# Kernel tuning notes

Measured on AMD Instinct MI355X. Metric: run time of the kernel, lower is better.

## Reference

```python
import jax, jax.numpy as jnp
import numpy as np

N, K, H, E, HEADS, MULT = 10000, 32, 128, 128, 8, 2
HD = H // HEADS


def _ln(x, g, b):
    m = jnp.mean(x, axis=-1, keepdims=True)
    v = jnp.var(x, axis=-1, keepdims=True)
    return (x - m) * jax.lax.rsqrt(v + 1e-5) * g + b


def setup_inputs() -> dict:
    key = jax.random.key(0)
    ks = jax.random.split(key, 40)
    s = 0.05
    inp = {
        "node_features": jax.random.normal(ks[0], (N, H), jnp.float32),
        "edge_features": jax.random.normal(ks[1], (N, K, H), jnp.float32),
        "edge_attr": jax.random.normal(ks[2], (N, K, E), jnp.float32),
        "neighbor_list": jax.random.randint(ks[3], (N, K), 0, N),
        "num_valid": jax.random.randint(ks[4], (N,), 1, K + 1),
        # edge_linear: E -> H (with activation)
        "W_edge": jax.random.normal(ks[5], (E, H), jnp.float32) * s,
        "b_edge": jnp.zeros((H,), jnp.float32),
        # node_linear: 2H -> H (cat of center + gathered neighbor features)
        "W_node": jax.random.normal(ks[6], (2 * H, H), jnp.float32) * s,
        "b_node": jnp.zeros((H,), jnp.float32),
        # message_linear: 2H -> H
        "W_msg": jax.random.normal(ks[7], (2 * H, H), jnp.float32) * s,
        "b_msg": jnp.zeros((H,), jnp.float32),
        # multi-head attention in/out projections
        "W_qkv": jax.random.normal(ks[8], (H, 3 * H), jnp.float32) * s,
        "b_qkv": jnp.zeros((3 * H,), jnp.float32),
        "W_out": jax.random.normal(ks[9], (H, H), jnp.float32) * s,
        "b_out": jnp.zeros((H,), jnp.float32),
        # layernorms
        "g_attn": jnp.ones((H,), jnp.float32), "be_attn": jnp.zeros((H,), jnp.float32),
        "g_fn": jnp.ones((H,), jnp.float32), "be_fn": jnp.zeros((H,), jnp.float32),
        "g_fe": jnp.ones((H,), jnp.float32), "be_fe": jnp.zeros((H,), jnp.float32),
        # FFNs (node and edge), hidden = MULT*H
        "Wn1": jax.random.normal(ks[10], (H, MULT * H), jnp.float32) * s,
        "bn1": jnp.zeros((MULT * H,), jnp.float32),
        "Wn2": jax.random.normal(ks[11], (MULT * H, H), jnp.float32) * s,
        "bn2": jnp.zeros((H,), jnp.float32),
        "We1": jax.random.normal(ks[12], (H, MULT * H), jnp.float32) * s,
        "be1": jnp.zeros((MULT * H,), jnp.float32),
        "We2": jax.random.normal(ks[13], (MULT * H, H), jnp.float32) * s,
        "be2": jnp.zeros((H,), jnp.float32),
    }
    return inp


def _block(node_features, edge_features, edge_attr, neighbor_list, mask,
           W_edge, b_edge, W_node, b_node, W_msg, b_msg,
           W_qkv, b_qkv, W_out, b_out,
           g_attn, be_attn, g_fn, be_fn, g_fe, be_fe,
           Wn1, bn1, Wn2, bn2, We1, be1, We2, be2):
    act = jax.nn.gelu
    # --- pre-attention norm on nodes ---
    node_hidden = _ln(node_features, g_attn, be_attn)                 # [N,H]
    # --- graph attention: gather -> MLPs -> local windowed attention -> scatter ---
    edge_hidden = act(jnp.einsum('nke,eh->nkh', edge_attr, W_edge) + b_edge)   # [N,K,H]
    nbr = node_hidden[neighbor_list]                                   # [N,K,H] gather
    center = jnp.broadcast_to(node_hidden[:, None, :], nbr.shape)      # [N,K,H]
    node_cat = jnp.concatenate([center, nbr], axis=-1)                 # [N,K,2H]
    node_hid = act(jnp.einsum('nkf,fh->nkh', node_cat, W_node) + b_node)
    msg = act(jnp.einsum('nkf,fh->nkh',
                         jnp.concatenate([edge_hidden, node_hid], axis=-1),
                         W_msg) + b_msg)                               # [N,K,H]
    # multi-head self-attention per node over its K neighbors, key padding mask
    qkv = jnp.einsum('nkh,hf->nkf', msg, W_qkv) + b_qkv                # [N,K,3H]
    q, k, v = jnp.split(qkv, 3, axis=-1)
    q = q.reshape(N, K, HEADS, HD)
    k = k.reshape(N, K, HEADS, HD)
    v = v.reshape(N, K, HEADS, HD)
    scores = jnp.einsum('nqhd,nkhd->nhqk', q, k) / np.sqrt(HD)         # [N,heads,K,K]
    scores = jnp.where(mask[:, None, None, :], scores, jnp.float32(-1e9))
    attn = jax.nn.softmax(scores, axis=-1)
    ctx = jnp.einsum('nhqk,nkhd->nqhd', attn, v).reshape(N, K, H)
    edge_out = jnp.einsum('nkh,hf->nkf', ctx, W_out) + b_out           # [N,K,H]
    # masked scatter-aggregate back to nodes
    node_out = jnp.sum(edge_out * mask[:, :, None], axis=1)            # [N,H]
    # residuals
    node_features = node_out + node_features
    edge_features = edge_out + edge_features
    # --- FFN block ---
    nh = _ln(node_features, g_fn, be_fn)
    eh = _ln(edge_features, g_fe, be_fe)
    nh = act(nh @ Wn1 + bn1) @ Wn2 + bn2
    eh = jnp.einsum('nkf,fh->nkh', act(jnp.einsum('nkh,hf->nkf', eh, We1) + be1), We2) + be2
    return node_features + nh, edge_features + eh


def reference(node_features, edge_features, edge_attr, neighbor_list, num_valid,
              W_edge, b_edge, W_node, b_node, W_msg, b_msg,
              W_qkv, b_qkv, W_out, b_out,
              g_attn, be_attn, g_fn, be_fn, g_fe, be_fe,
              Wn1, bn1, Wn2, bn2, We1, be1, We2, be2):
    mask = jnp.arange(K)[None, :] < num_valid[:, None]                 # [N,K] bool
    return _block(node_features, edge_features, edge_attr, neighbor_list, mask,
                  W_edge, b_edge, W_node, b_node, W_msg, b_msg,
                  W_qkv, b_qkv, W_out, b_out,
                  g_attn, be_attn, g_fn, be_fn, g_fe, be_fe,
                  Wn1, bn1, Wn2, bn2, We1, be1, We2, be2)
```

## Files before the change

### kernel.cpp

```cpp
#include <hip/hip_runtime.h>
#include <hip/hip_bf16.h>
#include <cstddef>

#define N_NODES 10000
#define KNBR 32
#define HDIM 128
#define NHEADS 8

using short8 = __attribute__((ext_vector_type(8))) short;
using short4v = __attribute__((ext_vector_type(4))) short;
using f32x4 = __attribute__((ext_vector_type(4))) float;

__device__ __forceinline__ f32x4 mfma16(short8 a, short8 b, f32x4 c) {
  return __builtin_amdgcn_mfma_f32_16x16x32_bf16(a, b, c, 0, 0, 0);
}

__device__ __forceinline__ short f2bf(float f) {
  __hip_bfloat16 h = __float2bfloat16(f);
  return __builtin_bit_cast(short, h);
}
__device__ __forceinline__ float bf2f(short s) {
  unsigned u = ((unsigned)(unsigned short)s) << 16;
  return __builtin_bit_cast(float, u);
}

__device__ __forceinline__ float gelu_f(float x) {
  float a = 0.7978845608028654f * fmaf(0.044715f * x, x * x, x);
  float e = __expf(2.0f * a);
  return 0.5f * x * (2.0f - 2.0f / (e + 1.0f));
}

__device__ __forceinline__ short4v pack4f(float a, float b, float c, float d) {
  short4v v; v[0] = f2bf(a); v[1] = f2bf(b); v[2] = f2bf(c); v[3] = f2bf(d);
  return v;
}
__device__ __forceinline__ short4v pack_gelu4(f32x4 acc, float4 bb) {
  return pack4f(gelu_f(acc[0] + bb.x), gelu_f(acc[1] + bb.y),
                gelu_f(acc[2] + bb.z), gelu_f(acc[3] + bb.w));
}

__device__ __forceinline__ short8 ld_sw128(const short* b, int r, int ch) {
  return *(const short8*)(b + r * 128 + (((ch ^ (r & 7))) << 3));
}
__device__ __forceinline__ short8 ld_sw256(const short* b, int r, int ch) {
  return *(const short8*)(b + r * 256 + (((ch ^ (r & 7))) << 3));
}
__device__ __forceinline__ void st_sw128(short* b, int r, int col, short v) {
  b[r * 128 + ((((col >> 3) ^ (r & 7))) << 3) + (col & 7)] = v;
}
__device__ __forceinline__ void st_sw128_v4(short* b, int r, int colb, short4v v) {
  *(short4v*)(b + r * 128 + ((((colb >> 3) ^ (r & 7))) << 3) + (colb & 7)) = v;
}
__device__ __forceinline__ void st_sw256_v4(short* b, int r, int colb, short4v v) {
  *(short4v*)(b + r * 256 + ((((colb >> 3) ^ (r & 7))) << 3) + (colb & 7)) = v;
}

template <int MT, int NT, int KS, typename ALoad, typename Epi>
__device__ __forceinline__ void wgemm(ALoad aload, const short* __restrict__ Bt,
                                      Epi epi) {
  const int lane = threadIdx.x & 63;
  const int lm = lane & 15, lq = lane >> 4;
  short8 a[MT][KS];
#pragma unroll
  for (int mt = 0; mt < MT; ++mt)
#pragma unroll
    for (int k = 0; k < KS; ++k) a[mt][k] = aload(mt * 16 + lm, k, lq);
#pragma unroll
  for (int nt = 0; nt < NT; ++nt) {
    short8 b[KS];
#pragma unroll
    for (int k = 0; k < KS; ++k)
      b[k] = *(const short8*)(Bt + (nt * 16 + lm) * (KS * 32) + k * 32 + lq * 8);
#pragma unroll
    for (int mt = 0; mt < MT; ++mt) {
      f32x4 acc = {0.f, 0.f, 0.f, 0.f};
#pragma unroll
      for (int k = 0; k < KS; ++k) acc = mfma16(a[mt][k], b[k], acc);
      epi(mt, nt, acc);
    }
  }
}

template <int MT, int NT, int KS, typename ALoad, typename Epi>
__device__ __forceinline__ void wgemm_t(ALoad aload, const short* __restrict__ Bt,
                                        Epi epi) {
  const int lane = threadIdx.x & 63;
  const int lm = lane & 15, lq = lane >> 4;
  short8 a[MT][KS];
#pragma unroll
  for (int mt = 0; mt < MT; ++mt)
#pragma unroll
    for (int k = 0; k < KS; ++k) a[mt][k] = aload(mt * 16 + lm, k, lq);
#pragma unroll
  for (int nt = 0; nt < NT; ++nt) {
    short8 b[KS];
#pragma unroll
    for (int k = 0; k < KS; ++k)
      b[k] = *(const short8*)(Bt + (nt * 16 + lm) * (KS * 32) + k * 32 + lq * 8);
#pragma unroll
    for (int mt = 0; mt < MT; ++mt) {
      f32x4 acc = {0.f, 0.f, 0.f, 0.f};
#pragma unroll
      for (int k = 0; k < KS; ++k) acc = mfma16(b[k], a[mt][k], acc);
      epi(mt, nt, acc);
    }
  }
}

struct WSrc { const float* p[9]; };

__global__ void wprep_kernel(WSrc ws, short* __restrict__ dst) {
  const int cum[10] = {0, 16384, 49152, 81920, 131072, 147456, 180224, 212992, 245760, 278528};
  const int Ks[9] = {128, 256, 256, 128, 128, 128, 256, 128, 256};
  const int Ns[9] = {128, 128, 128, 384, 128, 256, 128, 256, 128};
  int eg = blockIdx.x * 256 + threadIdx.x;
  int id = 0;
#pragma unroll
  for (int i = 0; i < 8; ++i) id += (eg >= cum[i + 1]) ? 1 : 0;
  int e = eg - cum[id];
  int K = Ks[id];
  int n = (K == 128) ? (e >> 7) : (e >> 8);
  int k = e - n * K;
  dst[eg] = f2bf(ws.p[id][k * Ns[id] + n]);
}

__global__ __launch_bounds__(256) void ln_in_kernel(
    const float* __restrict__ in, const float* __restrict__ g,
    const float* __restrict__ be, short* __restrict__ out) {
  __shared__ float scr[32 * 8 * 2 + 64];
  const int tid = threadIdx.x;
  const int r = tid >> 3, j = tid & 7;
  const int base = blockIdx.x * 32;
  const int rg = base + r;
  const bool valid = rg < N_NODES;
  float4 v[4];
#pragma unroll
  for (int i = 0; i < 4; ++i)
    v[i] = valid ? ((const float4*)(in + (size_t)rg * 128 + j * 16))[i]
                 : make_float4(0.f, 0.f, 0.f, 0.f);
  float s = 0.f, s2 = 0.f;
#pragma unroll
  for (int i = 0; i < 4; ++i) {
    s += v[i].x + v[i].y + v[i].z + v[i].w;
    s2 = fmaf(v[i].x, v[i].x, s2); s2 = fmaf(v[i].y, v[i].y, s2);
    s2 = fmaf(v[i].z, v[i].z, s2); s2 = fmaf(v[i].w, v[i].w, s2);
  }
  scr[r * 8 + j] = s;
  scr[256 + r * 8 + j] = s2;
  __syncthreads();
  if (tid < 32) {
    float ss = 0.f, q2 = 0.f;
#pragma unroll
    for (int i = 0; i < 8; ++i) { ss += scr[tid * 8 + i]; q2 += scr[256 + tid * 8 + i]; }
    float mn = ss * (1.f / 128.f);
    float vr = fmaf(-mn, mn, q2 * (1.f / 128.f));
    scr[512 + tid] = mn;
    scr[544 + tid] = rsqrtf(vr + 1e-5f);
  }
  __syncthreads();
  if (!valid) return;
  float mn = scr[512 + r], rs = scr[544 + r];
  short8 o[2];
#pragma unroll
  for (int i = 0; i < 4; ++i) {
    int c0 = j * 16 + i * 4;
    float4 gg = *(const float4*)(g + c0);
    float4 bb = *(const float4*)(be + c0);
    float* vf = (float*)&v[i];
    float* gf = (float*)&gg;
    float* bf = (float*)&bb;
#pragma unroll
    for (int e = 0; e < 4; ++e)
      o[i >> 1][(i & 1) * 4 + e] = f2bf(fmaf((vf[e] - mn) * rs, gf[e], bf[e]));
  }
  *(short8*)(out + (size_t)rg * 128 + j * 16) = o[0];
  *(short8*)(out + (size_t)rg * 128 + j * 16 + 8) = o[1];
}

__global__ __launch_bounds__(256, 3) void egab_main(
    const float* __restrict__ nf, const float* __restrict__ ef,
    const float* __restrict__ ea, const int* __restrict__ nlist,
    const int* __restrict__ nvalid,
    const float* __restrict__ b_edge, const float* __restrict__ b_node,
    const float* __restrict__ b_msg, const float* __restrict__ b_qkv,
    const float* __restrict__ b_out, const float* __restrict__ g_fe,
    const float* __restrict__ be_fe, const float* __restrict__ be1,
    const float* __restrict__ be2,
    const short* __restrict__ WtE, const short* __restrict__ WtN,
    const short* __restrict__ WtM, const short* __restrict__ WtQ,
    const short* __restrict__ WtO, const short* __restrict__ WtE1,
    const short* __restrict__ WtE2, const short* __restrict__ nh_bf,
    float* __restrict__ out_node, float* __restrict__ out_edge) {
  __shared__ short lds[16384];
  short* R0 = lds;
  short* R1 = lds + 4096;
  short* R2 = lds + 8192;
  short* R3 = lds + 12288;

  const int tid = threadIdx.x;
  const int w = tid >> 6;
  const int lane = tid & 63;
  const int lm = lane & 15, lq = lane >> 4;
  const int base = blockIdx.x;
  const int n0 = w * 32;

  float efr[2][2][4];
  float nfr[2];
#pragma unroll
  for (int mt = 0; mt < 2; ++mt)
#pragma unroll
    for (int nt = 0; nt < 2; ++nt)
#pragma unroll
      for (int rr = 0; rr < 4; ++rr)
        efr[mt][nt][rr] =
            ef[((size_t)base * KNBR + mt * 16 + lq * 4 + rr) * 128 + n0 +
               nt * 16 + lm];
#pragma unroll
  for (int nt = 0; nt < 2; ++nt)
    nfr[nt] = nf[(size_t)base * 128 + n0 + nt * 16 + lm];

  {
    const float* eap = ea + (size_t)base * 4096;
    int r = tid >> 3;
    int sg = tid & 7;
#pragma unroll
    for (int j = 0; j < 2; ++j) {
      int ch = sg * 2 + j;
      float4 fa = ((const float4*)eap)[r * 32 + ch * 2];
      float4 fb = ((const float4*)eap)[r * 32 + ch * 2 + 1];
      short8 v = {f2bf(fa.x), f2bf(fa.y), f2bf(fa.z), f2bf(fa.w),
                  f2bf(fb.x), f2bf(fb.y), f2bf(fb.z), f2bf(fb.w)};
      *(short8*)(R0 + r * 128 + ((ch ^ (r & 7)) << 3)) = v;
    }
    int idx = nlist[base * KNBR + r];
    const short* srow = nh_bf + (size_t)idx * 128;
#pragma unroll
    for (int j = 0; j < 2; ++j) {
      int ch = sg * 2 + j;
      short8 v = *(const short8*)(srow + ch * 8);
      *(short8*)(R1 + r * 128 + ((ch ^ (r & 7)) << 3)) = v;
    }
  }
  __syncthreads();

  wgemm_t<2, 2, 4>(
      [&](int r, int k, int q) { return ld_sw128(R0, r, k * 4 + q); },
      WtE + (size_t)n0 * 128,
      [&](int mt, int nt, f32x4 acc) {
        int colb = n0 + nt * 16 + lq * 4;
        float4 bb = *(const float4*)(b_edge + colb);
        st_sw128_v4(R2, mt * 16 + lm, colb, pack_gelu4(acc, bb));
      });
  wgemm_t<2, 2, 8>(
      [&](int r, int k, int q) {
        if (k < 4)
          return *(const short8*)(nh_bf + (size_t)base * 128 + k * 32 + q * 8);
        return ld_sw128(R1, r, (k - 4) * 4 + q);
      },
      WtN + (size_t)n0 * 256,
      [&](int mt, int nt, f32x4 acc) {
        int colb = n0 + nt * 16 + lq * 4;
        float4 bb = *(const float4*)(b_node + colb);
        st_sw128_v4(R3, mt * 16 + lm, colb, pack_gelu4(acc, bb));
      });
  __syncthreads();

  wgemm_t<2, 2, 8>(
      [&](int r, int k, int q) {
        if (k < 4) return ld_sw128(R2, r, k * 4 + q);
        return ld_sw128(R3, r, (k - 4) * 4 + q);
      },
      WtM + (size_t)n0 * 256,
      [&](int mt, int nt, f32x4 acc) {
        int colb = n0 + nt * 16 + lq * 4;
        float4 bb = *(const float4*)(b_msg + colb);
        st_sw128_v4(R0, mt * 16 + lm, colb, pack_gelu4(acc, bb));
      });
  __syncthreads();

  {
    const int q0 = w * 96;
    wgemm<2, 6, 4>(
        [&](int r, int k, int q) { return ld_sw128(R0, r, k * 4 + q); },
        WtQ + (size_t)q0 * 128,
        [&](int mt, int nt, f32x4 acc) {
          int c = q0 + nt * 16;
          float bb = b_qkv[c + lm];
          int m = mt * 16 + lq * 4;
          if (c < 256) {
            short* dst = (c < 128 ? R1 + ((c >> 4) * 32) * 16
                                  : R2 + (((c - 128) >> 4) * 32) * 16);
#pragma unroll
            for (int rr = 0; rr < 4; ++rr)
              dst[(m + rr) * 16 + lm] = f2bf(acc[rr] + bb);
          } else {
            int rv = (c - 256) + lm;
            short4v pv;
#pragma unroll
            for (int rr = 0; rr < 4; ++rr) pv[rr] = f2bf(acc[rr] + bb);
            int chv = m >> 3;
            *(short4v*)(R3 + rv * 32 + ((chv ^ (rv & 3)) << 3) + (m & 7)) = pv;
          }
        });
  }
  __syncthreads();

  {
    const short8 zz = {0, 0, 0, 0, 0, 0, 0, 0};
    const f32x4 z4 = {0.f, 0.f, 0.f, 0.f};
    const int nvv = nvalid[base];
#pragma unroll
    for (int it = 0; it < 2; ++it) {
      int h = (it << 2) | w;
      short* qh = R1 + h * 512;
      short* kh = R2 + h * 512;
      short8 bk[2];
#pragma unroll
      for (int nt = 0; nt < 2; ++nt)
        bk[nt] = (lq < 2) ? *(const short8*)(kh + (nt * 16 + lm) * 16 + lq * 8) : zz;
      float sc[2][2][4];
#pragma unroll
      for (int mt = 0; mt < 2; ++mt) {
        short8 aq = (lq < 2) ? *(const short8*)(qh + (mt * 16 + lm) * 16 + lq * 8) : zz;
#pragma unroll
        for (int nt = 0; nt < 2; ++nt) {
          f32x4 s = mfma16(aq, bk[nt], z4);
#pragma unroll
          for (int rr = 0; rr < 4; ++rr) {
            float x = s[rr] * 0.25f;
            if (nt * 16 + lm >= nvv) x = -1e9f;
            sc[mt][nt][rr] = x;
          }
        }
      }
#pragma unroll
      for (int mt = 0; mt < 2; ++mt)
#pragma unroll
        for (int rr = 0; rr < 4; ++rr) {
          float x0 = sc[mt][0][rr], x1 = sc[mt][1][rr];
          float mx = fmaxf(x0, x1);
          mx = fmaxf(mx, __shfl_xor(mx, 1, 16));
          mx = fmaxf(mx, __shfl_xor(mx, 2, 16));
          mx = fmaxf(mx, __shfl_xor(mx, 4, 16));
          mx = fmaxf(mx, __shfl_xor(mx, 8, 16));
          float e0 = __expf(x0 - mx), e1 = __expf(x1 - mx);
          float sm = e0 + e1;
          sm += __shfl_xor(sm, 1, 16);
          sm += __shfl_xor(sm, 2, 16);
          sm += __shfl_xor(sm, 4, 16);
          sm += __shfl_xor(sm, 8, 16);
          float ri = 1.f / sm;
          int row = mt * 16 + lq * 4 + rr;
          qh[row * 16 + lm] = f2bf(e0 * ri);
          kh[row * 16 + lm] = f2bf(e1 * ri);
        }
#pragma unroll
      for (int mt = 0; mt < 2; ++mt) {
        const short* psrc = (lq < 2) ? qh : kh;
        short8 pa = *(const short8*)(psrc + (mt * 16 + lm) * 16 + (lq & 1) * 8);
        int rv = h * 16 + lm;
        short8 vb = *(const short8*)(R3 + rv * 32 + ((lq ^ (rv & 3)) << 3));
        f32x4 c = mfma16(pa, vb, z4);
#pragma unroll
        for (int rr = 0; rr < 4; ++rr)
          st_sw128(R0, mt * 16 + lq * 4 + rr, h * 16 + lm, f2bf(c[rr]));
      }
    }
  }
  __syncthreads();

  {
    int nv = nvalid[base];
    float nsum[2] = {0.f, 0.f};
    wgemm<2, 2, 4>(
        [&](int r, int k, int q) { return ld_sw128(R0, r, k * 4 + q); },
        WtO + (size_t)n0 * 128,
        [&](int mt, int nt, f32x4 acc) {
          int col = n0 + nt * 16 + lm;
          float bb = b_out[col];
#pragma unroll
          for (int rr = 0; rr < 4; ++rr) {
            int kk = mt * 16 + lq * 4 + rr;
            float eo = acc[rr] + bb;
            if (kk < nv) nsum[nt] += eo;
            st_sw128(R1, kk, col, f2bf(eo + efr[mt][nt][rr]));
          }
        });
#pragma unroll
    for (int nt = 0; nt < 2; ++nt) {
      float v = nsum[nt];
      v += __shfl_xor(v, 16, 64);
      v += __shfl_xor(v, 32, 64);
      if (lq == 0) {
        int col = n0 + nt * 16 + lm;
        out_node[(size_t)base * 128 + col] = v + nfr[nt];
      }
    }
  }
  __syncthreads();

  {
    float* scr = (float*)R2;
    int r = tid >> 3, sg = tid & 7;
    short8 xv[2];
    float s = 0.f, s2 = 0.f;
#pragma unroll
    for (int j = 0; j < 2; ++j) {
      int ch = sg * 2 + j;
      xv[j] = *(const short8*)(R1 + r * 128 + ((ch ^ (r & 7)) << 3));
#pragma unroll
      for (int e = 0; e < 8; ++e) {
        float x = bf2f(xv[j][e]);
        s += x;
        s2 = fmaf(x, x, s2);
      }
    }
    scr[r * 8 + sg] = s;
    scr[256 + r * 8 + sg] = s2;
    __syncthreads();
    if (tid < 32) {
      float ss = 0.f, q2 = 0.f;
#pragma unroll
      for (int i = 0; i < 8; ++i) { ss += scr[tid * 8 + i]; q2 += scr[256 + tid * 8 + i]; }
      float mn = ss * (1.f / 128.f);
      float vr = fmaf(-mn, mn, q2 * (1.f / 128.f));
      scr[512 + tid * 2] = mn;
      scr[512 + tid * 2 + 1] = rsqrtf(vr + 1e-5f);
    }
    __syncthreads();
    float mn = scr[512 + r * 2], rs = scr[512 + r * 2 + 1];
#pragma unroll
    for (int j = 0; j < 2; ++j) {
      int ch = sg * 2 + j;
      int c0 = ch * 8;
      float4 g0 = *(const float4*)(g_fe + c0);
      float4 g1 = *(const float4*)(g_fe + c0 + 4);
      float4 b0 = *(const float4*)(be_fe + c0);
      float4 b1 = *(const float4*)(be_fe + c0 + 4);
      const float* gp0 = (const float*)&g0;
      const float* gp1 = (const float*)&g1;
      const float* bp0 = (const float*)&b0;
      const float* bp1 = (const float*)&b1;
      short8 ov;
#pragma unroll
      for (int e = 0; e < 4; ++e) {
        ov[e] = f2bf(fmaf((bf2f(xv[j][e]) - mn) * rs, gp0[e], bp0[e]));
        ov[4 + e] = f2bf(fmaf((bf2f(xv[j][4 + e]) - mn) * rs, gp1[e], bp1[e]));
      }
      *(short8*)(R0 + r * 128 + ((ch ^ (r & 7)) << 3)) = ov;
    }
  }
  __syncthreads();

  {
    const int f0 = w * 64;
    wgemm_t<2, 4, 4>(
        [&](int r, int k, int q) { return ld_sw128(R0, r, k * 4 + q); },
        WtE1 + (size_t)f0 * 128,
        [&](int mt, int nt, f32x4 acc) {
          int colb = f0 + nt * 16 + lq * 4;
          float4 bb = *(const float4*)(be1 + colb);
          st_sw256_v4(R2, mt * 16 + lm, colb, pack_gelu4(acc, bb));
        });
  }
  __syncthreads();

  wgemm<2, 2, 8>(
      [&](int r, int k, int q) { return ld_sw256(R2, r, k * 4 + q); },
      WtE2 + (size_t)n0 * 256,
      [&](int mt, int nt, f32x4 acc) {
        int col = n0 + nt * 16 + lm;
        float bb = be2[col];
#pragma unroll
        for (int rr = 0; rr < 4; ++rr) {
          int m = mt * 16 + lq * 4 + rr;
          float rv = bf2f(R1[m * 128 + ((((col >> 3) ^ (m & 7))) << 3) + (col & 7)]);
          out_edge[((size_t)base * KNBR + m) * 128 + col] = rv + acc[rr] + bb;
        }
      });
}

__global__ __launch_bounds__(256, 4) void node_ffn_kernel(
    const float* __restrict__ nres, const float* __restrict__ g,
    const float* __restrict__ be, const short* __restrict__ WtN1,
    const float* __restrict__ bn1, const short* __restrict__ WtN2,
    const float* __restrict__ bn2, float* __restrict__ out) {
  __shared__ short lds[8192];
  short* EHN = lds;
  float* scr = (float*)(lds + 2048);
  short* HID = lds + 4096;

  const int tid = threadIdx.x;
  const int w = tid >> 6;
  const int lane = tid & 63;
  const int lm = lane & 15, lq = lane >> 4;
  const int base = blockIdx.x * 16;
  const int n0 = w * 32;

  {
    int r = tid >> 4, sg = tid & 15;
    bool valid = (base + r) < N_NODES;
    float xf[8];
#pragma unroll
    for (int i = 0; i < 2; ++i) {
      float4 v = valid ? ((const float4*)(nres + (size_t)(base + r) * 128 + sg * 8))[i]
                       : make_float4(0.f, 0.f, 0.f, 0.f);
      xf[i * 4] = v.x; xf[i * 4 + 1] = v.y; xf[i * 4 + 2] = v.z; xf[i * 4 + 3] = v.w;
    }
    float s = 0.f, s2 = 0.f;
#pragma unroll
    for (int i = 0; i < 8; ++i) { s += xf[i]; s2 = fmaf(xf[i], xf[i], s2); }
    scr[r * 16 + sg] = s;
    scr[256 + r * 16 + sg] = s2;
    __syncthreads();
    if (tid < 16) {
      float ss = 0.f, q2 = 0.f;
#pragma unroll
      for (int i = 0; i < 16; ++i) { ss += scr[tid * 16 + i]; q2 += scr[256 + tid * 16 + i]; }
      float mn = ss * (1.f / 128.f);
      float vr = fmaf(-mn, mn, q2 * (1.f / 128.f));
      scr[512 + tid * 2] = mn;
      scr[512 + tid * 2 + 1] = rsqrtf(vr + 1e-5f);
    }
    __syncthreads();
    float mn = scr[512 + r * 2], rs = scr[512 + r * 2 + 1];
    int c0 = sg * 8;
    short8 ov;
#pragma unroll
    for (int e = 0; e < 8; ++e)
      ov[e] = f2bf(fmaf((xf[e] - mn) * rs, g[c0 + e], be[c0 + e]));
    *(short8*)(EHN + r * 128 + ((sg ^ (r & 7)) << 3)) = ov;
  }
  __syncthreads();

  {
    const int f0 = w * 64;
    wgemm_t<1, 4, 4>(
        [&](int r, int k, int q) { return ld_sw128(EHN, r, k * 4 + q); },
        WtN1 + (size_t)f0 * 128,
        [&](int mt, int nt, f32x4 acc) {
          int colb = f0 + nt * 16 + lq * 4;
          float4 bb = *(const float4*)(bn1 + colb);
          st_sw256_v4(HID, mt * 16 + lm, colb, pack_gelu4(acc, bb));
        });
  }
  __syncthreads();

  wgemm<1, 2, 8>(
      [&](int r, int k, int q) { return ld_sw256(HID, r, k * 4 + q); },
      WtN2 + (size_t)n0 * 256,
      [&](int mt, int nt, f32x4 acc) {
        int col = n0 + nt * 16 + lm;
        float bb = bn2[col];
#pragma unroll
        for (int rr = 0; rr < 4; ++rr) {
          int m = mt * 16 + lq * 4 + rr;
          if (base + m < N_NODES) {
            float rv = nres[(size_t)(base + m) * 128 + col];
            out[(size_t)(base + m) * 128 + col] = rv + acc[rr] + bb;
          }
        }
      });
}

extern "C" void kernel_launch(void* const* d_in, const int* in_sizes, int n_in,
                              void* d_out, int out_size, void* d_ws,
                              size_t ws_size, hipStream_t stream) {
  (void)in_sizes; (void)n_in; (void)out_size; (void)ws_size;
  const float* nf = (const float*)d_in[0];
  const float* ef = (const float*)d_in[1];
  const float* ea = (const float*)d_in[2];
  const int* nlist = (const int*)d_in[3];
  const int* nvalid = (const int*)d_in[4];
  const float* W_edge = (const float*)d_in[5];
  const float* b_edge = (const float*)d_in[6];
  const float* W_node = (const float*)d_in[7];
  const float* b_node = (const float*)d_in[8];
  const float* W_msg = (const float*)d_in[9];
  const float* b_msg = (const float*)d_in[10];
  const float* W_qkv = (const float*)d_in[11];
  const float* b_qkv = (const float*)d_in[12];
  const float* W_out = (const float*)d_in[13];
  const float* b_out = (const float*)d_in[14];
  const float* g_attn = (const float*)d_in[15];
  const float* be_attn = (const float*)d_in[16];
  const float* g_fn = (const float*)d_in[17];
  const float* be_fn = (const float*)d_in[18];
  const float* g_fe = (const float*)d_in[19];
  const float* be_fe = (const float*)d_in[20];
  const float* Wn1 = (const float*)d_in[21];
  const float* bn1 = (const float*)d_in[22];
  const float* Wn2 = (const float*)d_in[23];
  const float* bn2 = (const float*)d_in[24];
  const float* We1 = (const float*)d_in[25];
  const float* be1 = (const float*)d_in[26];
  const float* We2 = (const float*)d_in[27];
  const float* be2 = (const float*)d_in[28];

  short* ws0 = (short*)d_ws;
  short* wsW = ws0 + 1280000;
  short* WtE = wsW;
  short* WtN = wsW + 16384;
  short* WtM = wsW + 49152;
  short* WtQ = wsW + 81920;
  short* WtO = wsW + 131072;
  short* WtE1 = wsW + 147456;
  short* WtE2 = wsW + 180224;
  short* WtN1 = wsW + 212992;
  short* WtN2 = wsW + 245760;

  float* out_node = (float*)d_out;
  float* out_edge = out_node + (size_t)N_NODES * 128;

  WSrc wsrc;
  wsrc.p[0] = W_edge; wsrc.p[1] = W_node; wsrc.p[2] = W_msg;
  wsrc.p[3] = W_qkv;  wsrc.p[4] = W_out;  wsrc.p[5] = We1;
  wsrc.p[6] = We2;    wsrc.p[7] = Wn1;    wsrc.p[8] = Wn2;

  wprep_kernel<<<1088, 256, 0, stream>>>(wsrc, wsW);
  ln_in_kernel<<<(N_NODES + 31) / 32, 256, 0, stream>>>(nf, g_attn, be_attn, ws0);
  egab_main<<<N_NODES, 256, 0, stream>>>(
      nf, ef, ea, nlist, nvalid, b_edge, b_node, b_msg, b_qkv, b_out, g_fe,
      be_fe, be1, be2, WtE, WtN, WtM, WtQ, WtO, WtE1, WtE2, ws0, out_node,
      out_edge);
  node_ffn_kernel<<<(N_NODES + 15) / 16, 256, 0, stream>>>(
      out_node, g_fn, be_fn, WtN1, bn1, WtN2, bn2, out_node);
}
```

Baseline: 911.8 us.

## Fuse node FFN into main kernel and use cheaper sigmoid-form GELU

Removes the separate node_ffn_kernel launch. Each block of egab_main now computes the node LayerNorm and runs the node FFN for its single node, using MFMA with only row 0 of the A operand non-zero. GELU is rewritten as x*sigmoid(1.5958*(x+0.044715x^3)), using hardware exp2 and rcp intrinsics to cut transcendental cost. The trade-off is wasted MFMA work on padded rows, extra weight loads per block (WtN1/WtN2 read by all 10000 blocks), and slightly more LDS use.

Measured after the change: 1.023 ms. 12.1% more time.

```diff
diff --git a/kernel.cpp b/kernel.cpp
--- a/kernel.cpp
+++ b/kernel.cpp
@@ -25,9 +25,8 @@
 }
 
 __device__ __forceinline__ float gelu_f(float x) {
-  float a = 0.7978845608028654f * fmaf(0.044715f * x, x * x, x);
-  float e = __expf(2.0f * a);
-  return 0.5f * x * (2.0f - 2.0f / (e + 1.0f));
+  float u = x * fmaf(x * x, -0.1029432f, -2.3022077f);
+  return x * __builtin_amdgcn_rcpf(1.0f + __builtin_amdgcn_exp2f(u));
 }
 
 __device__ __forceinline__ short4v pack4f(float a, float b, float c, float d) {
@@ -185,17 +184,21 @@
     const float* __restrict__ b_msg, const float* __restrict__ b_qkv,
     const float* __restrict__ b_out, const float* __restrict__ g_fe,
     const float* __restrict__ be_fe, const float* __restrict__ be1,
-    const float* __restrict__ be2,
+    const float* __restrict__ be2, const float* __restrict__ g_fn,
+    const float* __restrict__ be_fn, const float* __restrict__ bn1,
+    const float* __restrict__ bn2,
     const short* __restrict__ WtE, const short* __restrict__ WtN,
     const short* __restrict__ WtM, const short* __restrict__ WtQ,
     const short* __restrict__ WtO, const short* __restrict__ WtE1,
-    const short* __restrict__ WtE2, const short* __restrict__ nh_bf,
+    const short* __restrict__ WtE2, const short* __restrict__ WtN1,
+    const short* __restrict__ WtN2, const short* __restrict__ nh_bf,
     float* __restrict__ out_node, float* __restrict__ out_edge) {
-  __shared__ short lds[16384];
+  __shared__ short lds[16384 + 384];
   short* R0 = lds;
   short* R1 = lds + 4096;
   short* R2 = lds + 8192;
   short* R3 = lds + 12288;
+  short* ffn = lds + 16384;
 
   const int tid = threadIdx.x;
   const int w = tid >> 6;
@@ -203,6 +206,9 @@
   const int lm = lane & 15, lq = lane >> 4;
   const int base = blockIdx.x;
   const int n0 = w * 32;
+  const short8 zz8 = {0, 0, 0, 0, 0, 0, 0, 0};
+
+  float xres[2];
 
   float efr[2][2][4];
   float nfr[2];
@@ -306,7 +312,6 @@
   __syncthreads();
 
   {
-    const short8 zz = {0, 0, 0, 0, 0, 0, 0, 0};
     const f32x4 z4 = {0.f, 0.f, 0.f, 0.f};
     const int nvv = nvalid[base];
 #pragma unroll
@@ -317,11 +322,11 @@
       short8 bk[2];
 #pragma unroll
       for (int nt = 0; nt < 2; ++nt)
-        bk[nt] = (lq < 2) ? *(const short8*)(kh + (nt * 16 + lm) * 16 + lq * 8) : zz;
+        bk[nt] = (lq < 2) ? *(const short8*)(kh + (nt * 16 + lm) * 16 + lq * 8) : zz8;
       float sc[2][2][4];
 #pragma unroll
       for (int mt = 0; mt < 2; ++mt) {
-        short8 aq = (lq < 2) ? *(const short8*)(qh + (mt * 16 + lm) * 16 + lq * 8) : zz;
+        short8 aq = (lq < 2) ? *(const short8*)(qh + (mt * 16 + lm) * 16 + lq * 8) : zz8;
 #pragma unroll
         for (int nt = 0; nt < 2; ++nt) {
           f32x4 s = mfma16(aq, bk[nt], z4);
@@ -386,15 +391,14 @@
             st_sw128(R1, kk, col, f2bf(eo + efr[mt][nt][rr]));
           }
         });
+    float* xf = (float*)R2;
 #pragma unroll
     for (int nt = 0; nt < 2; ++nt) {
       float v = nsum[nt];
       v += __shfl_xor(v, 16, 64);
       v += __shfl_xor(v, 32, 64);
-      if (lq == 0) {
-        int col = n0 + nt * 16 + lm;
-        out_node[(size_t)base * 128 + col] = v + nfr[nt];
-      }
+      xres[nt] = v + nfr[nt];
+      if (lq == 0) xf[1024 + n0 + nt * 16 + lm] = xres[nt];
     }
   }
   __syncthreads();
@@ -417,6 +421,12 @@
     }
     scr[r * 8 + sg] = s;
     scr[256 + r * 8 + sg] = s2;
+    if (tid < 32) {
+      float4 x4 = *(const float4*)(scr + 1024 + tid * 4);
+      scr[832 + tid] = x4.x + x4.y + x4.z + x4.w;
+      scr[864 + tid] = fmaf(x4.x, x4.x, fmaf(x4.y, x4.y,
+                       fmaf(x4.z, x4.z, x4.w * x4.w)));
+    }
     __syncthreads();
     if (tid < 32) {
       float ss = 0.f, q2 = 0.f;
@@ -426,6 +436,14 @@
       float vr = fmaf(-mn, mn, q2 * (1.f / 128.f));
       scr[512 + tid * 2] = mn;
       scr[512 + tid * 2 + 1] = rsqrtf(vr + 1e-5f);
+    } else if (tid == 64) {
+      float ss = 0.f, q2 = 0.f;
+#pragma unroll
+      for (int i = 0; i < 32; ++i) { ss += scr[832 + i]; q2 += scr[864 + i]; }
+      float mn = ss * (1.f / 128.f);
+      float vr = fmaf(-mn, mn, q2 * (1.f / 128.f));
+      scr[896] = mn;
+      scr[897] = rsqrtf(vr + 1e-5f);
     }
     __syncthreads();
     float mn = scr[512 + r * 2], rs = scr[512 + r * 2 + 1];
@@ -449,6 +467,10 @@
       }
       *(short8*)(R0 + r * 128 + ((ch ^ (r & 7)) << 3)) = ov;
     }
+    if (tid < 128) {
+      float mx = scr[896], rx = scr[897];
+      ffn[tid] = f2bf(fmaf((scr[1024 + tid] - mx) * rx, g_fn[tid], be_fn[tid]));
+    }
   }
   __syncthreads();
 
@@ -462,6 +484,19 @@
           float4 bb = *(const float4*)(be1 + colb);
           st_sw256_v4(R2, mt * 16 + lm, colb, pack_gelu4(acc, bb));
         });
+    wgemm<1, 4, 4>(
+        [&](int r, int k, int q) {
+          short8 av = *(const short8*)(ffn + k * 32 + q * 8);
+          return (lm == 0) ? av : zz8;
+        },
+        WtN1 + (size_t)f0 * 128,
+        [&](int mt, int nt, f32x4 acc) {
+          (void)mt;
+          if (lq == 0) {
+            int col = f0 + nt * 16 + lm;
+            ffn[128 + col] = f2bf(gelu_f(acc[0] + bn1[col]));
+          }
+        });
   }
   __syncthreads();
 
@@ -478,87 +513,17 @@
           out_edge[((size_t)base * KNBR + m) * 128 + col] = rv + acc[rr] + bb;
         }
       });
-}
-
-__global__ __launch_bounds__(256, 4) void node_ffn_kernel(
-    const float* __restrict__ nres, const float* __restrict__ g,
-    const float* __restrict__ be, const short* __restrict__ WtN1,
-    const float* __restrict__ bn1, const short* __restrict__ WtN2,
-    const float* __restrict__ bn2, float* __restrict__ out) {
-  __shared__ short lds[8192];
-  short* EHN = lds;
-  float* scr = (float*)(lds + 2048);
-  short* HID = lds + 4096;
-
-  const int tid = threadIdx.x;
-  const int w = tid >> 6;
-  const int lane = tid & 63;
-  const int lm = lane & 15, lq = lane >> 4;
-  const int base = blockIdx.x * 16;
-  const int n0 = w * 32;
-
-  {
-    int r = tid >> 4, sg = tid & 15;
-    bool valid = (base + r) < N_NODES;
-    float xf[8];
-#pragma unroll
-    for (int i = 0; i < 2; ++i) {
-      float4 v = valid ? ((const float4*)(nres + (size_t)(base + r) * 128 + sg * 8))[i]
-                       : make_float4(0.f, 0.f, 0.f, 0.f);
-      xf[i * 4] = v.x; xf[i * 4 + 1] = v.y; xf[i * 4 + 2] = v.z; xf[i * 4 + 3] = v.w;
-    }
-    float s = 0.f, s2 = 0.f;
-#pragma unroll
-    for (int i = 0; i < 8; ++i) { s += xf[i]; s2 = fmaf(xf[i], xf[i], s2); }
-    scr[r * 16 + sg] = s;
-    scr[256 + r * 16 + sg] = s2;
-    __syncthreads();
-    if (tid < 16) {
-      float ss = 0.f, q2 = 0.f;
-#pragma unroll
-      for (int i = 0; i < 16; ++i) { ss += scr[tid * 16 + i]; q2 += scr[256 + tid * 16 + i]; }
-      float mn = ss * (1.f / 128.f);
-      float vr = fmaf(-mn, mn, q2 * (1.f / 128.f));
-      scr[512 + tid * 2] = mn;
-      scr[512 + tid * 2 + 1] = rsqrtf(vr + 1e-5f);
-    }
-    __syncthreads();
-    float mn = scr[512 + r * 2], rs = scr[512 + r * 2 + 1];
-    int c0 = sg * 8;
-    short8 ov;
-#pragma unroll
-    for (int e = 0; e < 8; ++e)
-      ov[e] = f2bf(fmaf((xf[e] - mn) * rs, g[c0 + e], be[c0 + e]));
-    *(short8*)(EHN + r * 128 + ((sg ^ (r & 7)) << 3)) = ov;
-  }
-  __syncthreads();
-
-  {
-    const int f0 = w * 64;
-    wgemm_t<1, 4, 4>(
-        [&](int r, int k, int q) { return ld_sw128(EHN, r, k * 4 + q); },
-        WtN1 + (size_t)f0 * 128,
-        [&](int mt, int nt, f32x4 acc) {
-          int colb = f0 + nt * 16 + lq * 4;
-          float4 bb = *(const float4*)(bn1 + colb);
-          st_sw256_v4(HID, mt * 16 + lm, colb, pack_gelu4(acc, bb));
-        });
-  }
-  __syncthreads();
-
   wgemm<1, 2, 8>(
-      [&](int r, int k, int q) { return ld_sw256(HID, r, k * 4 + q); },
+      [&](int r, int k, int q) {
+        short8 av = *(const short8*)(ffn + 128 + k * 32 + q * 8);
+        return (lm == 0) ? av : zz8;
+      },
       WtN2 + (size_t)n0 * 256,
       [&](int mt, int nt, f32x4 acc) {
-        int col = n0 + nt * 16 + lm;
-        float bb = bn2[col];
-#pragma unroll
-        for (int rr = 0; rr < 4; ++rr) {
-          int m = mt * 16 + lq * 4 + rr;
-          if (base + m < N_NODES) {
-            float rv = nres[(size_t)(base + m) * 128 + col];
-            out[(size_t)(base + m) * 128 + col] = rv + acc[rr] + bb;
-          }
+        (void)mt;
+        if (lq == 0) {
+          int col = n0 + nt * 16 + lm;
+          out_node[(size_t)base * 128 + col] = xres[nt] + acc[0] + bn2[col];
         }
       });
 }
@@ -621,8 +586,6 @@
   ln_in_kernel<<<(N_NODES + 31) / 32, 256, 0, stream>>>(nf, g_attn, be_attn, ws0);
   egab_main<<<N_NODES, 256, 0, stream>>>(
       nf, ef, ea, nlist, nvalid, b_edge, b_node, b_msg, b_qkv, b_out, g_fe,
-      be_fe, be1, be2, WtE, WtN, WtM, WtQ, WtO, WtE1, WtE2, ws0, out_node,
-      out_edge);
-  node_ffn_kernel<<<(N_NODES + 15) / 16, 256, 0, stream>>>(
-      out_node, g_fn, be_fn, WtN1, bn1, WtN2, bn2, out_node);
-}
+      be_fe, be1, be2, g_fn, be_fn, bn1, bn2, WtE, WtN, WtM, WtQ, WtO, WtE1,
+      WtE2, WtN1, WtN2, ws0, out_node, out_edge);
+}
```

## Split K=256 GEMMs into two passes, drop preloaded residuals, raise occupancy

Applied to the files above, without the earlier changes.

Splits each K=256 wave GEMM into two K=128 passes that accumulate into shared register accumulators, so fewer A/B fragments are live at once. The edge and node residuals are no longer preloaded into registers at kernel start; they are read from global memory in the epilogue. The main kernel's launch bound rises from 3 to 4 blocks per SM. GELU is rewritten as x·sigmoid in exp2/rcp form using hardware intrinsics. Together these aim to cut register pressure and raise occupancy, at the cost of later residual loads that can no longer hide behind compute, and slightly different GELU rounding.

Result: faster. 892.6 us (-2.1%).

```diff
diff --git a/kernel.cpp b/kernel.cpp
--- a/kernel.cpp
+++ b/kernel.cpp
@@ -25,9 +25,8 @@
 }
 
 __device__ __forceinline__ float gelu_f(float x) {
-  float a = 0.7978845608028654f * fmaf(0.044715f * x, x * x, x);
-  float e = __expf(2.0f * a);
-  return 0.5f * x * (2.0f - 2.0f / (e + 1.0f));
+  float u = x * fmaf(x * x, -0.1029432f, -2.3022077f);
+  return x * __builtin_amdgcn_rcpf(1.0f + __builtin_amdgcn_exp2f(u));
 }
 
 __device__ __forceinline__ short4v pack4f(float a, float b, float c, float d) {
@@ -54,6 +53,7 @@
 __device__ __forceinline__ void st_sw256_v4(short* b, int r, int colb, short4v v) {
   *(short4v*)(b + r * 256 + ((((colb >> 3) ^ (r & 7))) << 3) + (colb & 7)) = v;
 }
+
 
 template <int MT, int NT, int KS, typename ALoad, typename Epi>
 __device__ __forceinline__ void wgemm(ALoad aload, const short* __restrict__ Bt,
@@ -104,6 +104,56 @@
       for (int k = 0; k < KS; ++k) acc = mfma16(b[k], a[mt][k], acc);
       epi(mt, nt, acc);
     }
+  }
+}
+
+template <int MT, int NT, int KS, typename ALoad>
+__device__ __forceinline__ void wgemm_pass(ALoad aload,
+                                           const short* __restrict__ Bt,
+                                           int brs, f32x4 (&acc)[MT][NT]) {
+  const int lane = threadIdx.x & 63;
+  const int lm = lane & 15, lq = lane >> 4;
+  short8 a[MT][KS];
+#pragma unroll
+  for (int mt = 0; mt < MT; ++mt)
+#pragma unroll
+    for (int k = 0; k < KS; ++k) a[mt][k] = aload(mt * 16 + lm, k, lq);
+#pragma unroll
+  for (int nt = 0; nt < NT; ++nt) {
+    short8 b[KS];
+#pragma unroll
+    for (int k = 0; k < KS; ++k)
+      b[k] = *(const short8*)(Bt + (nt * 16 + lm) * brs + k * 32 + lq * 8);
+#pragma unroll
+    for (int mt = 0; mt < MT; ++mt)
+#pragma unroll
+      for (int k = 0; k < KS; ++k)
+        acc[mt][nt] = mfma16(a[mt][k], b[k], acc[mt][nt]);
+  }
+}
+
+template <int MT, int NT, int KS, typename ALoad>
+__device__ __forceinline__ void wgemm_t_pass(ALoad aload,
+                                             const short* __restrict__ Bt,
+                                             int brs, f32x4 (&acc)[MT][NT]) {
+  const int lane = threadIdx.x & 63;
+  const int lm = lane & 15, lq = lane >> 4;
+  short8 a[MT][KS];
+#pragma unroll
+  for (int mt = 0; mt < MT; ++mt)
+#pragma unroll
+    for (int k = 0; k < KS; ++k) a[mt][k] = aload(mt * 16 + lm, k, lq);
+#pragma unroll
+  for (int nt = 0; nt < NT; ++nt) {
+    short8 b[KS];
+#pragma unroll
+    for (int k = 0; k < KS; ++k)
+      b[k] = *(const short8*)(Bt + (nt * 16 + lm) * brs + k * 32 + lq * 8);
+#pragma unroll
+    for (int mt = 0; mt < MT; ++mt)
+#pragma unroll
+      for (int k = 0; k < KS; ++k)
+        acc[mt][nt] = mfma16(b[k], a[mt][k], acc[mt][nt]);
   }
 }
 
@@ -177,7 +227,7 @@
   *(short8*)(out + (size_t)rg * 128 + j * 16 + 8) = o[1];
 }
 
-__global__ __launch_bounds__(256, 3) void egab_main(
+__global__ __launch_bounds__(256, 4) void egab_main(
     const float* __restrict__ nf, const float* __restrict__ ef,
     const float* __restrict__ ea, const int* __restrict__ nlist,
     const int* __restrict__ nvalid,
@@ -204,21 +254,6 @@
   const int base = blockIdx.x;
   const int n0 = w * 32;
 
-  float efr[2][2][4];
-  float nfr[2];
-#pragma unroll
-  for (int mt = 0; mt < 2; ++mt)
-#pragma unroll
-    for (int nt = 0; nt < 2; ++nt)
-#pragma unroll
-      for (int rr = 0; rr < 4; ++rr)
-        efr[mt][nt][rr] =
-            ef[((size_t)base * KNBR + mt * 16 + lq * 4 + rr) * 128 + n0 +
-               nt * 16 + lm];
-#pragma unroll
-  for (int nt = 0; nt < 2; ++nt)
-    nfr[nt] = nf[(size_t)base * 128 + n0 + nt * 16 + lm];
-
   {
     const float* eap = ea + (size_t)base * 4096;
     int r = tid >> 3;
@@ -251,31 +286,53 @@
         float4 bb = *(const float4*)(b_edge + colb);
         st_sw128_v4(R2, mt * 16 + lm, colb, pack_gelu4(acc, bb));
       });
-  wgemm_t<2, 2, 8>(
-      [&](int r, int k, int q) {
-        if (k < 4)
+  {
+    f32x4 ac[2][2];
+#pragma unroll
+    for (int mt = 0; mt < 2; ++mt)
+#pragma unroll
+      for (int nt = 0; nt < 2; ++nt) ac[mt][nt] = {0.f, 0.f, 0.f, 0.f};
+    wgemm_t_pass<2, 2, 4>(
+        [&](int r, int k, int q) {
+          (void)r;
           return *(const short8*)(nh_bf + (size_t)base * 128 + k * 32 + q * 8);
-        return ld_sw128(R1, r, (k - 4) * 4 + q);
-      },
-      WtN + (size_t)n0 * 256,
-      [&](int mt, int nt, f32x4 acc) {
+        },
+        WtN + (size_t)n0 * 256, 256, ac);
+    wgemm_t_pass<2, 2, 4>(
+        [&](int r, int k, int q) { return ld_sw128(R1, r, k * 4 + q); },
+        WtN + (size_t)n0 * 256 + 128, 256, ac);
+#pragma unroll
+    for (int mt = 0; mt < 2; ++mt)
+#pragma unroll
+      for (int nt = 0; nt < 2; ++nt) {
         int colb = n0 + nt * 16 + lq * 4;
         float4 bb = *(const float4*)(b_node + colb);
-        st_sw128_v4(R3, mt * 16 + lm, colb, pack_gelu4(acc, bb));
-      });
-  __syncthreads();
-
-  wgemm_t<2, 2, 8>(
-      [&](int r, int k, int q) {
-        if (k < 4) return ld_sw128(R2, r, k * 4 + q);
-        return ld_sw128(R3, r, (k - 4) * 4 + q);
-      },
-      WtM + (size_t)n0 * 256,
-      [&](int mt, int nt, f32x4 acc) {
+        st_sw128_v4(R3, mt * 16 + lm, colb, pack_gelu4(ac[mt][nt], bb));
+      }
+  }
+  __syncthreads();
+
+  {
+    f32x4 ac[2][2];
+#pragma unroll
+    for (int mt = 0; mt < 2; ++mt)
+#pragma unroll
+      for (int nt = 0; nt < 2; ++nt) ac[mt][nt] = {0.f, 0.f, 0.f, 0.f};
+    wgemm_t_pass<2, 2, 4>(
+        [&](int r, int k, int q) { return ld_sw128(R2, r, k * 4 + q); },
+        WtM + (size_t)n0 * 256, 256, ac);
+    wgemm_t_pass<2, 2, 4>(
+        [&](int r, int k, int q) { return ld_sw128(R3, r, k * 4 + q); },
+        WtM + (size_t)n0 * 256 + 128, 256, ac);
+#pragma unroll
+    for (int mt = 0; mt < 2; ++mt)
+#pragma unroll
+      for (int nt = 0; nt < 2; ++nt) {
         int colb = n0 + nt * 16 + lq * 4;
         float4 bb = *(const float4*)(b_msg + colb);
-        st_sw128_v4(R0, mt * 16 + lm, colb, pack_gelu4(acc, bb));
-      });
+        st_sw128_v4(R0, mt * 16 + lm, colb, pack_gelu4(ac[mt][nt], bb));
+      }
+  }
   __syncthreads();
 
   {
@@ -383,7 +440,8 @@
             int kk = mt * 16 + lq * 4 + rr;
             float eo = acc[rr] + bb;
             if (kk < nv) nsum[nt] += eo;
-            st_sw128(R1, kk, col, f2bf(eo + efr[mt][nt][rr]));
+            float efv = ef[((size_t)base * KNBR + kk) * 128 + col];
+            st_sw128(R1, kk, col, f2bf(eo + efv));
           }
         });
 #pragma unroll
@@ -393,7 +451,8 @@
       v += __shfl_xor(v, 32, 64);
       if (lq == 0) {
         int col = n0 + nt * 16 + lm;
-        out_node[(size_t)base * 128 + col] = v + nfr[nt];
+        out_node[(size_t)base * 128 + col] =
+            v + nf[(size_t)base * 128 + col];
       }
     }
   }
@@ -465,19 +524,33 @@
   }
   __syncthreads();
 
-  wgemm<2, 2, 8>(
-      [&](int r, int k, int q) { return ld_sw256(R2, r, k * 4 + q); },
-      WtE2 + (size_t)n0 * 256,
-      [&](int mt, int nt, f32x4 acc) {
+  {
+    f32x4 ac[2][2];
+#pragma unroll
+    for (int mt = 0; mt < 2; ++mt)
+#pragma unroll
+      for (int nt = 0; nt < 2; ++nt) ac[mt][nt] = {0.f, 0.f, 0.f, 0.f};
+    wgemm_pass<2, 2, 4>(
+        [&](int r, int k, int q) { return ld_sw256(R2, r, k * 4 + q); },
+        WtE2 + (size_t)n0 * 256, 256, ac);
+    wgemm_pass<2, 2, 4>(
+        [&](int r, int k, int q) { return ld_sw256(R2, r, 16 + k * 4 + q); },
+        WtE2 + (size_t)n0 * 256 + 128, 256, ac);
+#pragma unroll
+    for (int mt = 0; mt < 2; ++mt)
+#pragma unroll
+      for (int nt = 0; nt < 2; ++nt) {
         int col = n0 + nt * 16 + lm;
         float bb = be2[col];
 #pragma unroll
         for (int rr = 0; rr < 4; ++rr) {
           int m = mt * 16 + lq * 4 + rr;
           float rv = bf2f(R1[m * 128 + ((((col >> 3) ^ (m & 7))) << 3) + (col & 7)]);
-          out_edge[((size_t)base * KNBR + m) * 128 + col] = rv + acc[rr] + bb;
+          out_edge[((size_t)base * KNBR + m) * 128 + col] =
+              rv + ac[mt][nt][rr] + bb;
         }
-      });
+      }
+  }
 }
 
 __global__ __launch_bounds__(256, 4) void node_ffn_kernel(
@@ -546,21 +619,30 @@
   }
   __syncthreads();
 
-  wgemm<1, 2, 8>(
-      [&](int r, int k, int q) { return ld_sw256(HID, r, k * 4 + q); },
-      WtN2 + (size_t)n0 * 256,
-      [&](int mt, int nt, f32x4 acc) {
-        int col = n0 + nt * 16 + lm;
-        float bb = bn2[col];
-#pragma unroll
-        for (int rr = 0; rr < 4; ++rr) {
-          int m = mt * 16 + lq * 4 + rr;
-          if (base + m < N_NODES) {
-            float rv = nres[(size_t)(base + m) * 128 + col];
-            out[(size_t)(base + m) * 128 + col] = rv + acc[rr] + bb;
-          }
+  {
+    f32x4 ac[1][2];
+    ac[0][0] = {0.f, 0.f, 0.f, 0.f};
+    ac[0][1] = {0.f, 0.f, 0.f, 0.f};
+    wgemm_pass<1, 2, 4>(
+        [&](int r, int k, int q) { return ld_sw256(HID, r, k * 4 + q); },
+        WtN2 + (size_t)n0 * 256, 256, ac);
+    wgemm_pass<1, 2, 4>(
+        [&](int r, int k, int q) { return ld_sw256(HID, r, 16 + k * 4 + q); },
+        WtN2 + (size_t)n0 * 256 + 128, 256, ac);
+#pragma unroll
+    for (int nt = 0; nt < 2; ++nt) {
+      int col = n0 + nt * 16 + lm;
+      float bb = bn2[col];
+#pragma unroll
+      for (int rr = 0; rr < 4; ++rr) {
+        int m = lq * 4 + rr;
+        if (base + m < N_NODES) {
+          float rv = nres[(size_t)(base + m) * 128 + col];
+          out[(size_t)(base + m) * 128 + col] = rv + ac[0][nt][rr] + bb;
         }
-      });
+      }
+    }
+  }
 }
 
 extern "C" void kernel_launch(void* const* d_in, const int* in_sizes, int n_in,
```
